# Kernel tuning notes

Hardware: AMD Instinct MI355X
Metric: run time of the kernel (lower is better)

Reference implementation:

```python
import jax, jax.numpy as jnp
import numpy as np

B, N, NTYPES, MN = 8, 1024, 2, 128
M = NTYPES * MN
BETA, M1, M2 = 8, 16, 4
NFEAT = M1 * M2
H = 128
NGHOST = 64
RMAX, RMIN = 6.0, 0.5
ENER_SHIFT = np.array([[-93.0], [-13.6]], dtype=np.float32)


def setup_inputs() -> dict:
    key = jax.random.key(0)
    ks = jax.random.split(key, 12)
    # displacement vectors with |r| in (1, Rmax-0.2)
    d = jax.random.normal(ks[0], (B, N, M, 3), jnp.float32)
    d = d / jnp.linalg.norm(d, axis=-1, keepdims=True)
    r = jax.random.uniform(ks[1], (B, N, M, 1), jnp.float32, 1.0, RMAX - 0.2)
    rvec = d * r
    list_neigh = jax.random.randint(ks[2], (B, N, NTYPES, MN), 1, N + NGHOST + 1).astype(jnp.int32)
    # sorted type map so per-type concat order matches original atom order
    Imagetype_map = jnp.concatenate([jnp.zeros(N // 2, jnp.int32), jnp.ones(N - N // 2, jnp.int32)])
    c_param = 0.1 * jax.random.normal(ks[3], (NTYPES, NTYPES, M1, BETA), jnp.float32)
    def w(k, shape):
        fan_in = shape[-2]
        return (1.0 / np.sqrt(fan_in)) * jax.random.normal(k, shape, jnp.float32)
    return {
        'list_neigh': list_neigh,
        'Imagetype_map': Imagetype_map,
        'rvec': rvec,
        'c_param': c_param,
        'W0': w(ks[4], (NTYPES, NFEAT, H)), 'b0': jnp.zeros((NTYPES, H), jnp.float32),
        'W1': w(ks[5], (NTYPES, H, H)),     'b1': jnp.zeros((NTYPES, H), jnp.float32),
        'W2': w(ks[6], (NTYPES, H, H)),     'b2': jnp.zeros((NTYPES, H), jnp.float32),
        'Wout': w(ks[7], (NTYPES, H, 1)),   'bout': jnp.asarray(ENER_SHIFT),
    }


def _cheb(u):
    # Chebyshev polynomials T_0..T_{BETA-1}, stacked on last axis
    Ts = [jnp.ones_like(u), u]
    for _ in range(2, BETA):
        Ts.append(2.0 * u * Ts[-1] - Ts[-2])
    return jnp.stack(Ts[:BETA], axis=-1)


def _features(rvec, Imagetype_map, c_param):
    r = jnp.linalg.norm(rvec, axis=-1)                      # (B,N,M)
    valid = r > 1e-6
    r_safe = jnp.where(valid, r, 1.0)
    span = RMAX - RMIN
    u = jnp.clip(2.0 * (r_safe - RMIN) / span - 1.0, -1.0, 1.0)
    fc = jnp.where(valid & (r_safe < RMAX),
                   0.5 * (jnp.cos(jnp.pi * (jnp.clip(r_safe, RMIN, RMAX) - RMIN) / span) + 1.0),
                   0.0)
    T = _cheb(u)                                            # (B,N,M,BETA)
    # per-pair Chebyshev coefficients c[type_i, type_j, m1, k]; neighbor type is the block index
    c_i = c_param[Imagetype_map]                            # (N, NTYPES, M1, BETA)
    c_pair = jnp.repeat(c_i, MN, axis=1)                    # (N, M, M1, BETA)
    g = jnp.einsum('bnmk,nmpk->bnmp', T, c_pair) * fc[..., None]   # (B,N,M,M1)
    unit = rvec / r_safe[..., None]
    q = jnp.concatenate([jnp.ones_like(r_safe)[..., None], unit], axis=-1)  # (B,N,M,4)
    q = q * valid[..., None]
    S = jnp.einsum('bnmp,bnma->bnpa', g, q) / M             # (B,N,M1,4)
    feat = jnp.einsum('bnpa,bnqa->bnpq', S, S[:, :, :M2])   # (B,N,M1,M2)
    return feat.reshape(feat.shape[0], feat.shape[1], NFEAT)


def _normalize(feat, Imagetype_map):
    # per-type StandardScaler over all feat values of atoms of that type (detached)
    means, stds = [], []
    for t in range(NTYPES):
        w = (Imagetype_map == t).astype(feat.dtype)         # (N,)
        cnt = w.sum() * feat.shape[0] * NFEAT
        mu = (feat * w[None, :, None]).sum() / cnt
        var = (((feat - mu) ** 2) * w[None, :, None]).sum() / (cnt - 1.0)
        means.append(mu)
        stds.append(jnp.sqrt(var))
    means = jax.lax.stop_gradient(jnp.stack(means))
    stds = jax.lax.stop_gradient(jnp.stack(stds))
    mt = means[Imagetype_map][None, :, None]
    st = stds[Imagetype_map][None, :, None]
    return (feat - mt) / st


def _fit(feat_n, Imagetype_map, W0, b0, W1, b1, W2, b2, Wout, bout):
    Ei = jnp.zeros(feat_n.shape[:2] + (1,), feat_n.dtype)
    for t in range(NTYPES):
        h = jnp.tanh(feat_n @ W0[t] + b0[t])
        h = jnp.tanh(h @ W1[t] + b1[t]) + h                 # resnet skip (equal dims)
        h = jnp.tanh(h @ W2[t] + b2[t]) + h
        e = h @ Wout[t] + bout[t]                           # (B,N,1)
        Ei = Ei + e * (Imagetype_map == t)[None, :, None]
    return Ei


def reference(list_neigh, Imagetype_map, rvec, c_param, W0, b0, W1, b1, W2, b2, Wout, bout):
    def ei_fn(rv):
        feat = _features(rv, Imagetype_map, c_param)
        feat_n = _normalize(feat, Imagetype_map)
        return _fit(feat_n, Imagetype_map, W0, b0, W1, b1, W2, b2, Wout, bout)

    Ei = ei_fn(rvec)                                        # (B,N,1)
    Etot = Ei.sum(axis=1)                                   # (B,1)

    # forces / virial: dE/d rij, scatter-add to center & neighbor atoms (incl. ghosts)
    dEdr = jax.grad(lambda rv: ei_fn(rv).sum())(rvec)       # (B,N,M,3)
    Force = jnp.zeros((B, N + NGHOST, 3), rvec.dtype)
    Force = Force.at[:, :N].add(dEdr.sum(axis=2))           # center atoms: F_i = +sum_j dE/drij
    nl = list_neigh.reshape(B, N, M)
    valid = nl > 0
    j = jnp.where(valid, nl - 1, 0)
    flat_idx = (jnp.arange(B)[:, None, None] * (N + NGHOST) + j).reshape(-1)
    contrib = jnp.where(valid[..., None], -dEdr, 0.0).reshape(-1, 3)
    Force = Force.reshape(-1, 3).at[flat_idx].add(contrib).reshape(B, N + NGHOST, 3)
    Virial = -jnp.einsum('bnma,bnmc->bac', rvec, dEdr).reshape(B, 9)
    return (Etot, Ei.squeeze(-1), Force, Virial)
```

## Files before the change

kernel.cpp:

```cpp
#include <hip/hip_runtime.h>
#include <math.h>

#define BB 8
#define NN 1024
#define MM 256
#define BETA 8
#define M1 16
#define NFEAT 64
#define HH 128
#define NTOT 1088
#define F3 (NTOT*3)
#define RMINf 0.5f
#define SPANf 5.5f
#define PIf 3.14159265358979323846f

#define OUT_EI 8
#define OUT_FORCE 8200
#define OUT_VIR 34312

#define NG2 128
#define AT2 (NN/NG2)

#define MT 16
#define AS0 68
#define AS1 132

#define FEAT_BLKS 2048

#define WS_S     0
#define WS_DF    (WS_S + 8192*64)
#define WS_FP    (WS_DF + 8192*64)
#define WS_STATP (WS_FP + BB*NG2*F3)
#define WS_VIRP  (WS_STATP + 8192*2)
#define WS_WTB   (WS_VIRP + BB*NG2*9)
#define WS_WB    (WS_WTB + 40960)
#define WT0_OFF  0
#define WT1_OFF  16384
#define WT2_OFF  49152

typedef __attribute__((ext_vector_type(8))) short bf8;
typedef __attribute__((ext_vector_type(4))) float f4;

__device__ __forceinline__ float ftanh(float x) {
  const float e = __expf(2.0f*x);
  return 1.0f - 2.0f/(e + 1.0f);
}
__device__ __forceinline__ short f2bs(float f) {
  unsigned u = __float_as_uint(f);
  return (short)((u + 0x7FFFu + ((u >> 16) & 1u)) >> 16);
}
__device__ __forceinline__ bf8 a_frag(const float* p) {
  bf8 a;
  #pragma unroll
  for (int i = 0; i < 8; ++i) a[i] = f2bs(p[i]);
  return a;
}
__device__ __forceinline__ f4 splat4(float v) {
  f4 r; r[0] = v; r[1] = v; r[2] = v; r[3] = v; return r;
}
__device__ __forceinline__ float dpp_wave_sum(float x) {
  x += __int_as_float(__builtin_amdgcn_update_dpp(0, __float_as_int(x), 0x111, 0xf, 0xf, true));
  x += __int_as_float(__builtin_amdgcn_update_dpp(0, __float_as_int(x), 0x112, 0xf, 0xf, true));
  x += __int_as_float(__builtin_amdgcn_update_dpp(0, __float_as_int(x), 0x114, 0xf, 0xf, true));
  x += __int_as_float(__builtin_amdgcn_update_dpp(0, __float_as_int(x), 0x118, 0xf, 0xf, true));
  x += __int_as_float(__builtin_amdgcn_update_dpp(0, __float_as_int(x), 0x142, 0xf, 0xf, true));
  x += __int_as_float(__builtin_amdgcn_update_dpp(0, __float_as_int(x), 0x143, 0xf, 0xf, true));
  return x;
}

__global__ __launch_bounds__(256) void k_feat(
    const float* __restrict__ rvec, const int* __restrict__ tmap,
    const float* __restrict__ c_param, float* __restrict__ S_ws,
    float* __restrict__ statp,
    const float* __restrict__ W0, const float* __restrict__ W1,
    const float* __restrict__ W2,
    unsigned short* __restrict__ wtb, unsigned short* __restrict__ wb)
{
  const int tid = threadIdx.x;
  if (blockIdx.x >= FEAT_BLKS) {
    const int idx = (blockIdx.x - FEAT_BLKS)*256 + tid;
    if (idx < 81920) {
      unsigned short v;
      if (idx < 16384) {
        const int t = idx >> 13, rem = idx & 8191;
        const int j = rem >> 6, f = rem & 63;
        v = (unsigned short)f2bs(W0[t*8192 + f*128 + j]);
      } else if (idx < 49152) {
        const int i = idx - 16384;
        const int t = i >> 14, rem = i & 16383;
        const int j = rem >> 7, f = rem & 127;
        v = (unsigned short)f2bs(W1[t*16384 + f*128 + j]);
      } else {
        const int i = idx - 49152;
        const int t = i >> 14, rem = i & 16383;
        const int j = rem >> 7, f = rem & 127;
        v = (unsigned short)f2bs(W2[t*16384 + f*128 + j]);
      }
      wtb[idx] = v;
    } else {
      const int k = idx - 81920;
      float src;
      if (k < 16384) src = W0[k];
      else if (k < 49152) src = W1[k - 16384];
      else src = W2[k - 49152];
      wb[k] = (unsigned short)f2bs(src);
    }
    return;
  }
  __shared__ float cA[512];
  __shared__ float Ubuf[4*64];
  __shared__ float Slds[4*64];
  cA[tid] = c_param[tid];
  cA[256 + tid] = c_param[256 + tid];
  __syncthreads();

  const int wave = tid >> 6, lane = tid & 63;
  const int bn = blockIdx.x*4 + wave;
  const int n = bn & (NN-1);
  const int ti = tmap[n];
  const float* rb = rvec + (size_t)bn*MM*3;

  #pragma unroll
  for (int half = 0; half < 2; ++half) {
    float acc[32];
    #pragma unroll
    for (int c = 0; c < 32; ++c) acc[c] = 0.f;
    #pragma unroll
    for (int s = 0; s < 2; ++s) {
      const int m = half*128 + s*64 + lane;
      const float x = rb[3*m], y = rb[3*m+1], z = rb[3*m+2];
      const float r = sqrtf(x*x + y*y + z*z);
      const float ir = 1.0f/r;
      const float ux = x*ir, uy = y*ir, uz = z*ir;
      float u = 2.0f*(r - RMINf)/SPANf - 1.0f;
      u = fminf(fmaxf(u, -1.0f), 1.0f);
      const float fc = 0.5f*(__cosf(PIf*(r - RMINf)/SPANf) + 1.0f);
      float tm2 = 1.0f, tm1 = u;
      acc[0] += fc;  acc[1] += fc*ux;  acc[2] += fc*uy;  acc[3] += fc*uz;
      {
        const float ft = fc*u;
        acc[4] += ft; acc[5] += ft*ux; acc[6] += ft*uy; acc[7] += ft*uz;
      }
      #pragma unroll
      for (int k = 2; k < BETA; ++k) {
        const float tk = 2.0f*u*tm1 - tm2;
        const float ft = fc*tk;
        acc[k*4+0] += ft;
        acc[k*4+1] += ft*ux;
        acc[k*4+2] += ft*uy;
        acc[k*4+3] += ft*uz;
        tm2 = tm1; tm1 = tk;
      }
    }
    #pragma unroll
    for (int c = 0; c < 32; ++c) acc[c] = dpp_wave_sum(acc[c]);
    if (lane == 63) {
      float* Uw = &Ubuf[wave*64 + half*32];
      #pragma unroll
      for (int c = 0; c < 32; ++c) Uw[c] = acc[c];
    }
  }
  {
    const int p = lane >> 2, a = lane & 3;
    const float* Uw = &Ubuf[wave*64];
    const float* cw = &cA[ti*256];
    float s = 0.f;
    #pragma unroll
    for (int tj = 0; tj < 2; ++tj)
      #pragma unroll
      for (int k = 0; k < 8; ++k)
        s += cw[tj*128 + p*8 + k] * Uw[tj*32 + k*4 + a];
    s *= (1.0f/(float)MM);
    Slds[wave*64 + lane] = s;
    S_ws[(size_t)bn*64 + lane] = s;
  }
  {
    const int p = lane >> 2, q = lane & 3;
    const float* Sw = &Slds[wave*64];
    float f = 0.f;
    #pragma unroll
    for (int a = 0; a < 4; ++a) f += Sw[p*4+a]*Sw[q*4+a];
    float fs = f, fss = f*f;
    for (int o = 32; o > 0; o >>= 1) { fs += __shfl_down(fs, o); fss += __shfl_down(fss, o); }
    if (lane == 0) { statp[bn*2+0] = fs; statp[bn*2+1] = fss; }
  }
}

__global__ __launch_bounds__(256) void k_mlp(
    const float* __restrict__ S_ws, const int* __restrict__ tmap,
    const float* __restrict__ statp,
    const unsigned short* __restrict__ wtb, const unsigned short* __restrict__ wb,
    const float* __restrict__ b0, const float* __restrict__ b1,
    const float* __restrict__ b2, const float* __restrict__ Wout,
    const float* __restrict__ bout,
    float* __restrict__ dfeat_ws, float* __restrict__ out)
{
  __shared__ float sl[MT*64];
  __shared__ float xb[MT*AS0];
  __shared__ float t0b[MT*AS1];
  __shared__ float h1b[MT*AS1];
  __shared__ float dzb[MT*AS1];
  __shared__ float es[MT];
  __shared__ float srd[8];
  __shared__ float muSd[2];
  const int tb = blockIdx.x;
  const int bn0 = tb*MT;
  const int tid = threadIdx.x;
  const int wave = tid >> 6, lane = tid & 63;
  const int quad = lane >> 4, nI = lane & 15;
  const int t = tmap[bn0 & (NN-1)];
  {
    const float4* src = (const float4*)(S_ws + (size_t)bn0*64);
    ((float4*)sl)[tid] = src[tid];
  }
  {
    float fs = 0.f, fss = 0.f;
    #pragma unroll 4
    for (int i = 0; i < 16; ++i) {
      const int e = i*256 + tid;
      const int b = e >> 9;
      const int n = t*512 + (e & 511);
      const float2 v = *(const float2*)&statp[((size_t)(b*NN + n))*2];
      fs += v.x; fss += v.y;
    }
    for (int o = 32; o > 0; o >>= 1) { fs += __shfl_down(fs, o); fss += __shfl_down(fss, o); }
    if ((tid & 63) == 0) { srd[(tid>>6)*2] = fs; srd[(tid>>6)*2+1] = fss; }
  }
  __syncthreads();
  if (tid == 0) {
    const float S1 = srd[0]+srd[2]+srd[4]+srd[6];
    const float S2 = srd[1]+srd[3]+srd[5]+srd[7];
    const float cnt = 512.0f * (float)BB * (float)NFEAT;
    const float mu = S1/cnt;
    const float var = (S2 - cnt*mu*mu)/(cnt - 1.0f);
    muSd[0] = mu; muSd[1] = sqrtf(fmaxf(var, 1e-20f));
  }
  __syncthreads();
  const float mu = muSd[0];
  const float inv_sd = 1.0f/muSd[1];
  #pragma unroll
  for (int i = 0; i < 4; ++i) {
    const int e = i*256 + tid;
    const int at = e >> 6, f = e & 63;
    const int p = f >> 2, q = f & 3;
    const float* Sr = &sl[at*64];
    float s = 0.f;
    #pragma unroll
    for (int a = 0; a < 4; ++a) s += Sr[p*4+a]*Sr[q*4+a];
    xb[at*AS0 + f] = (s - mu)*inv_sd;
  }
  __syncthreads();

  const int c0 = (wave*2+0)*16 + nI;
  const int c1 = (wave*2+1)*16 + nI;
  f4 acc0, acc1;

  acc0 = splat4(b0[t*HH + c0]);
  acc1 = splat4(b0[t*HH + c1]);
  {
    const unsigned short* B = wtb + WT0_OFF + t*8192;
    #pragma unroll
    for (int s = 0; s < 2; ++s) {
      const bf8 a  = a_frag(&xb[nI*AS0 + s*32 + quad*8]);
      const bf8 bA = *(const bf8*)&B[(size_t)c0*64 + s*32 + quad*8];
      const bf8 bB = *(const bf8*)&B[(size_t)c1*64 + s*32 + quad*8];
      acc0 = __builtin_amdgcn_mfma_f32_16x16x32_bf16(a, bA, acc0, 0, 0, 0);
      acc1 = __builtin_amdgcn_mfma_f32_16x16x32_bf16(a, bB, acc1, 0, 0, 0);
    }
  }
  #pragma unroll
  for (int r = 0; r < 4; ++r) {
    const int row = quad*4 + r;
    t0b[row*AS1 + c0] = ftanh(acc0[r]);
    t0b[row*AS1 + c1] = ftanh(acc1[r]);
  }
  __syncthreads();
  acc0 = splat4(b1[t*HH + c0]);
  acc1 = splat4(b1[t*HH + c1]);
  {
    const unsigned short* B = wtb + WT1_OFF + t*16384;
    #pragma unroll
    for (int s = 0; s < 4; ++s) {
      const bf8 a  = a_frag(&t0b[nI*AS1 + s*32 + quad*8]);
      const bf8 bA = *(const bf8*)&B[(size_t)c0*128 + s*32 + quad*8];
      const bf8 bB = *(const bf8*)&B[(size_t)c1*128 + s*32 + quad*8];
      acc0 = __builtin_amdgcn_mfma_f32_16x16x32_bf16(a, bA, acc0, 0, 0, 0);
      acc1 = __builtin_amdgcn_mfma_f32_16x16x32_bf16(a, bB, acc1, 0, 0, 0);
    }
  }
  #pragma unroll
  for (int r = 0; r < 4; ++r) {
    const int row = quad*4 + r;
    h1b[row*AS1 + c0] = ftanh(acc0[r]) + t0b[row*AS1 + c0];
    h1b[row*AS1 + c1] = ftanh(acc1[r]) + t0b[row*AS1 + c1];
  }
  __syncthreads();
  acc0 = splat4(b2[t*HH + c0]);
  acc1 = splat4(b2[t*HH + c1]);
  {
    const unsigned short* B = wtb + WT2_OFF + t*16384;
    #pragma unroll
    for (int s = 0; s < 4; ++s) {
      const bf8 a  = a_frag(&h1b[nI*AS1 + s*32 + quad*8]);
      const bf8 bA = *(const bf8*)&B[(size_t)c0*128 + s*32 + quad*8];
      const bf8 bB = *(const bf8*)&B[(size_t)c1*128 + s*32 + quad*8];
      acc0 = __builtin_amdgcn_mfma_f32_16x16x32_bf16(a, bA, acc0, 0, 0, 0);
      acc1 = __builtin_amdgcn_mfma_f32_16x16x32_bf16(a, bB, acc1, 0, 0, 0);
    }
  }
  #pragma unroll
  for (int r = 0; r < 4; ++r) {
    const int row = quad*4 + r;
    dzb[row*AS1 + c0] = acc0[r];
    dzb[row*AS1 + c1] = acc1[r];
  }
  __syncthreads();
  {
    const int at = tid >> 4, cb = (tid & 15)*8;
    const float* wop = Wout + t*HH;
    float ep = 0.f;
    #pragma unroll
    for (int j = 0; j < 8; ++j) {
      const int c = cb + j;
      const float z2 = dzb[at*AS1 + c];
      const float t2 = ftanh(z2);
      const float wo = wop[c];
      ep += (t2 + h1b[at*AS1 + c])*wo;
      dzb[at*AS1 + c] = wo*(1.0f - t2*t2);
    }
    ep += __shfl_down(ep, 8, 16);
    ep += __shfl_down(ep, 4, 16);
    ep += __shfl_down(ep, 2, 16);
    ep += __shfl_down(ep, 1, 16);
    if ((tid & 15) == 0) es[at] = ep;
  }
  __syncthreads();
  if (tid < MT) out[OUT_EI + bn0 + tid] = es[tid] + bout[t];

  {
    const float* wop = Wout + t*HH;
    acc0 = splat4(wop[c0]);
    acc1 = splat4(wop[c1]);
    const unsigned short* B = wb + WT2_OFF + t*16384;
    #pragma unroll
    for (int s = 0; s < 4; ++s) {
      const bf8 a  = a_frag(&dzb[nI*AS1 + s*32 + quad*8]);
      const bf8 bA = *(const bf8*)&B[(size_t)c0*128 + s*32 + quad*8];
      const bf8 bB = *(const bf8*)&B[(size_t)c1*128 + s*32 + quad*8];
      acc0 = __builtin_amdgcn_mfma_f32_16x16x32_bf16(a, bA, acc0, 0, 0, 0);
      acc1 = __builtin_amdgcn_mfma_f32_16x16x32_bf16(a, bB, acc1, 0, 0, 0);
    }
  }
  __syncthreads();
  float dh10[4], dh11[4];
  #pragma unroll
  for (int r = 0; r < 4; ++r) {
    const int row = quad*4 + r;
    dh10[r] = acc0[r]; dh11[r] = acc1[r];
    const float t1a = h1b[row*AS1 + c0] - t0b[row*AS1 + c0];
    const float t1b = h1b[row*AS1 + c1] - t0b[row*AS1 + c1];
    dzb[row*AS1 + c0] = acc0[r]*(1.0f - t1a*t1a);
    dzb[row*AS1 + c1] = acc1[r]*(1.0f - t1b*t1b);
  }
  __syncthreads();
  acc0[0]=dh10[0]; acc0[1]=dh10[1]; acc0[2]=dh10[2]; acc0[3]=dh10[3];
  acc1[0]=dh11[0]; acc1[1]=dh11[1]; acc1[2]=dh11[2]; acc1[3]=dh11[3];
  {
    const unsigned short* B = wb + WT1_OFF + t*16384;
    #pragma unroll
    for (int s = 0; s < 4; ++s) {
      const bf8 a  = a_frag(&dzb[nI*AS1 + s*32 + quad*8]);
      const bf8 bA = *(const bf8*)&B[(size_t)c0*128 + s*32 + quad*8];
      const bf8 bB = *(const bf8*)&B[(size_t)c1*128 + s*32 + quad*8];
      acc0 = __builtin_amdgcn_mfma_f32_16x16x32_bf16(a, bA, acc0, 0, 0, 0);
      acc1 = __builtin_amdgcn_mfma_f32_16x16x32_bf16(a, bB, acc1, 0, 0, 0);
    }
  }
  __syncthreads();
  #pragma unroll
  for (int r = 0; r < 4; ++r) {
    const int row = quad*4 + r;
    const float ta = t0b[row*AS1 + c0], tb = t0b[row*AS1 + c1];
    dzb[row*AS1 + c0] = acc0[r]*(1.0f - ta*ta);
    dzb[row*AS1 + c1] = acc1[r]*(1.0f - tb*tb);
  }
  __syncthreads();
  {
    const int cx = wave*16 + nI;
    acc0 = splat4(0.f);
    const unsigned short* B = wb + WT0_OFF + t*8192;
    #pragma unroll
    for (int s = 0; s < 4; ++s) {
      const bf8 a  = a_frag(&dzb[nI*AS1 + s*32 + quad*8]);
      const bf8 bA = *(const bf8*)&B[(size_t)cx*128 + s*32 + quad*8];
      acc0 = __builtin_amdgcn_mfma_f32_16x16x32_bf16(a, bA, acc0, 0, 0, 0);
    }
    #pragma unroll
    for (int r = 0; r < 4; ++r)
      dfeat_ws[(size_t)(bn0 + quad*4 + r)*64 + cx] = acc0[r]*inv_sd;
  }
}

__global__ __launch_bounds__(256, 4) void k_bwdsc(
    const float* __restrict__ rvec, const int* __restrict__ nlist,
    const int* __restrict__ tmap, const float* __restrict__ c_param,
    const float* __restrict__ S_ws, const float* __restrict__ dfeat_ws,
    float* __restrict__ fpart_ws, float* __restrict__ virp)
{
  __shared__ float c_lds[256];
  __shared__ float Sb[AT2*64];
  __shared__ float Db[AT2*64];
  __shared__ float dSb[AT2*64];
  __shared__ float Eb[AT2*64];
  __shared__ float fpart[F3];
  __shared__ float wredc[AT2*4*3];
  __shared__ float vred[4*9];
  const int blk = blockIdx.x;
  const int b = blk >> 7;
  const int g = blk & (NG2-1);
  const int n0 = g*AT2;
  const int tid = threadIdx.x;
  const int ti = tmap[n0];
  c_lds[tid] = c_param[ti*256 + tid];
  if (tid < 128) {
    const float4* s4 = (const float4*)(S_ws + ((size_t)b*NN + n0)*64);
    const float4* d4 = (const float4*)(dfeat_ws + ((size_t)b*NN + n0)*64);
    ((float4*)Sb)[tid] = s4[tid];
    ((float4*)Db)[tid] = d4[tid];
  }
  {
    const float4 z4 = {0.f, 0.f, 0.f, 0.f};
    for (int i = tid; i < F3/4; i += 256) ((float4*)fpart)[i] = z4;
  }
  __syncthreads();
  #pragma unroll
  for (int it = 0; it < 2; ++it) {
    const int idx = it*256 + tid;
    const int at = idx >> 6, f = idx & 63;
    const int i = f >> 2, a = f & 3;
    const float* Sr = &Sb[at*64];
    const float* Dr = &Db[at*64];
    float v = 0.f;
    #pragma unroll
    for (int q = 0; q < 4; ++q) v += Dr[i*4+q]*Sr[q*4+a];
    if (i < 4)
      for (int p = 0; p < 16; ++p) v += Dr[p*4+i]*Sr[p*4+a];
    dSb[idx] = v;
  }
  __syncthreads();
  #pragma unroll
  for (int it = 0; it < 2; ++it) {
    const int idx = it*256 + tid;
    const int at = idx >> 6, rem = idx & 63;
    const int tj = rem >> 5, a = (rem >> 3) & 3, k = rem & 7;
    float e = 0.f;
    #pragma unroll
    for (int p = 0; p < 16; ++p) e += dSb[at*64 + p*4 + a]*c_lds[tj*128 + p*8 + k];
    Eb[idx] = e;
  }
  __syncthreads();

  float vir[9];
  #pragma unroll
  for (int i = 0; i < 9; ++i) vir[i] = 0.f;
  const int wave = tid >> 6, lane = tid & 63;
  const int tjm = tid >> 7;
  const float dudr = 2.0f/SPANf;
  const float invM = 1.0f/(float)MM;

  const size_t rowbase = ((size_t)b*NN + n0)*MM;
  float px0, py0, pz0, px1, py1, pz1; int pnl0, pnl1;
  {
    const float* rp0 = rvec + (rowbase + tid)*3;
    const float* rp1 = rvec + (rowbase + MM + tid)*3;
    px0 = rp0[0]; py0 = rp0[1]; pz0 = rp0[2]; pnl0 = nlist[rowbase + tid];
    px1 = rp1[0]; py1 = rp1[1]; pz1 = rp1[2]; pnl1 = nlist[rowbase + MM + tid];
  }
  for (int a0 = 0; a0 < AT2; a0 += 2) {
    const float x0 = px0, y0 = py0, z0 = pz0; const int nl0 = pnl0;
    const float x1 = px1, y1 = py1, z1 = pz1; const int nl1 = pnl1;
    if (a0 + 2 < AT2) {
      const float* rp0 = rvec + (rowbase + (size_t)(a0+2)*MM + tid)*3;
      const float* rp1 = rvec + (rowbase + (size_t)(a0+3)*MM + tid)*3;
      px0 = rp0[0]; py0 = rp0[1]; pz0 = rp0[2];
      pnl0 = nlist[rowbase + (size_t)(a0+2)*MM + tid];
      px1 = rp1[0]; py1 = rp1[1]; pz1 = rp1[2];
      pnl1 = nlist[rowbase + (size_t)(a0+3)*MM + tid];
    }
    float Er0[32], Er1[32];
    {
      const float4* p0 = (const float4*)&Eb[a0*64 + tjm*32];
      const float4* p1 = (const float4*)&Eb[(a0+1)*64 + tjm*32];
      #pragma unroll
      for (int q = 0; q < 8; ++q) {
        const float4 v0 = p0[q], v1 = p1[q];
        Er0[q*4+0]=v0.x; Er0[q*4+1]=v0.y; Er0[q*4+2]=v0.z; Er0[q*4+3]=v0.w;
        Er1[q*4+0]=v1.x; Er1[q*4+1]=v1.y; Er1[q*4+2]=v1.z; Er1[q*4+3]=v1.w;
      }
    }
    const float r_0 = sqrtf(x0*x0 + y0*y0 + z0*z0);
    const float r_1 = sqrtf(x1*x1 + y1*y1 + z1*z1);
    const float ir0 = 1.0f/r_0, ir1 = 1.0f/r_1;
    const float ux0 = x0*ir0, uy0 = y0*ir0, uz0 = z0*ir0;
    const float ux1 = x1*ir1, uy1 = y1*ir1, uz1 = z1*ir1;
    float u0 = 2.0f*(r_0 - RMINf)/SPANf - 1.0f;
    float u1 = 2.0f*(r_1 - RMINf)/SPANf - 1.0f;
    u0 = fminf(fmaxf(u0, -1.0f), 1.0f);
    u1 = fminf(fmaxf(u1, -1.0f), 1.0f);
    float s0a, c0a, s1a, c1a;
    __sincosf(PIf*(r_0 - RMINf)/SPANf, &s0a, &c0a);
    __sincosf(PIf*(r_1 - RMINf)/SPANf, &s1a, &c1a);
    const float fc0 = 0.5f*(c0a + 1.0f), dfc0 = -0.5f*(PIf/SPANf)*s0a;
    const float fc1 = 0.5f*(c1a + 1.0f), dfc1 = -0.5f*(PIf/SPANf)*s1a;
    float ta0[4], tda0[4], ta1[4], tda1[4];
    #pragma unroll
    for (int aa = 0; aa < 4; ++aa) {
      ta0[aa]  = Er0[aa*8] + Er0[aa*8+1]*u0;
      tda0[aa] = Er0[aa*8+1];
      ta1[aa]  = Er1[aa*8] + Er1[aa*8+1]*u1;
      tda1[aa] = Er1[aa*8+1];
    }
    float t0m2 = 1.f, t0m1 = u0, d0m2 = 0.f, d0m1 = 1.f;
    float t1m2 = 1.f, t1m1 = u1, d1m2 = 0.f, d1m1 = 1.f;
    #pragma unroll
    for (int k = 2; k < BETA; ++k) {
      const float tk0 = 2.f*u0*t0m1 - t0m2;
      const float dk0 = 2.f*t0m1 + 2.f*u0*d0m1 - d0m2;
      const float tk1 = 2.f*u1*t1m1 - t1m2;
      const float dk1 = 2.f*t1m1 + 2.f*u1*d1m1 - d1m2;
      #pragma unroll
      for (int aa = 0; aa < 4; ++aa) {
        ta0[aa]  += Er0[aa*8+k]*tk0;
        tda0[aa] += Er0[aa*8+k]*dk0;
        ta1[aa]  += Er1[aa*8+k]*tk1;
        tda1[aa] += Er1[aa*8+k]*dk1;
      }
      t0m2 = t0m1; t0m1 = tk0; d0m2 = d0m1; d0m1 = dk0;
      t1m2 = t1m1; t1m1 = tk1; d1m2 = d1m1; d1m1 = dk1;
    }
    float A0 = dfc0*(ta0[0] + ux0*ta0[1] + uy0*ta0[2] + uz0*ta0[3])
             + fc0*dudr*(tda0[0] + ux0*tda0[1] + uy0*tda0[2] + uz0*tda0[3]);
    float A1 = dfc1*(ta1[0] + ux1*ta1[1] + uy1*ta1[2] + uz1*ta1[3])
             + fc1*dudr*(tda1[0] + ux1*tda1[1] + uy1*tda1[2] + uz1*tda1[3]);
    float q10 = fc0*ta0[1], q20 = fc0*ta0[2], q30 = fc0*ta0[3];
    float q11 = fc1*ta1[1], q21 = fc1*ta1[2], q31 = fc1*ta1[3];
    A0 *= invM; q10 *= invM; q20 *= invM; q30 *= invM;
    A1 *= invM; q11 *= invM; q21 *= invM; q31 *= invM;
    const float qu0 = q10*ux0 + q20*uy0 + q30*uz0;
    const float qu1 = q11*ux1 + q21*uy1 + q31*uz1;
    const float d00 = A0*ux0 + (q10 - qu0*ux0)*ir0;
    const float d01 = A0*uy0 + (q20 - qu0*uy0)*ir0;
    const float d02 = A0*uz0 + (q30 - qu0*uz0)*ir0;
    const float d10 = A1*ux1 + (q11 - qu1*ux1)*ir1;
    const float d11 = A1*uy1 + (q21 - qu1*uy1)*ir1;
    const float d12 = A1*uz1 + (q31 - qu1*uz1)*ir1;
    if (nl0 > 0) {
      const int j = nl0 - 1;
      atomicAdd(&fpart[j*3+0], -d00);
      atomicAdd(&fpart[j*3+1], -d01);
      atomicAdd(&fpart[j*3+2], -d02);
    }
    if (nl1 > 0) {
      const int j = nl1 - 1;
      atomicAdd(&fpart[j*3+0], -d10);
      atomicAdd(&fpart[j*3+1], -d11);
      atomicAdd(&fpart[j*3+2], -d12);
    }
    vir[0] -= x0*d00 + x1*d10; vir[1] -= x0*d01 + x1*d11; vir[2] -= x0*d02 + x1*d12;
    vir[3] -= y0*d00 + y1*d10; vir[4] -= y0*d01 + y1*d11; vir[5] -= y0*d02 + y1*d12;
    vir[6] -= z0*d00 + z1*d10; vir[7] -= z0*d01 + z1*d11; vir[8] -= z0*d02 + z1*d12;
    const float r00 = dpp_wave_sum(d00), r01 = dpp_wave_sum(d01), r02 = dpp_wave_sum(d02);
    const float r10 = dpp_wave_sum(d10), r11 = dpp_wave_sum(d11), r12 = dpp_wave_sum(d12);
    if (lane == 63) {
      wredc[(a0*4 + wave)*3 + 0] = r00;
      wredc[(a0*4 + wave)*3 + 1] = r01;
      wredc[(a0*4 + wave)*3 + 2] = r02;
      wredc[((a0+1)*4 + wave)*3 + 0] = r10;
      wredc[((a0+1)*4 + wave)*3 + 1] = r11;
      wredc[((a0+1)*4 + wave)*3 + 2] = r12;
    }
  }
  #pragma unroll
  for (int i = 0; i < 9; ++i) {
    const float v = dpp_wave_sum(vir[i]);
    if (lane == 63) vred[wave*9 + i] = v;
  }
  __syncthreads();
  if (tid < AT2*3) {
    const int at = tid/3, c = tid - at*3;
    const float v = wredc[(at*4+0)*3+c] + wredc[(at*4+1)*3+c]
                  + wredc[(at*4+2)*3+c] + wredc[(at*4+3)*3+c];
    atomicAdd(&fpart[(n0+at)*3 + c], v);
  }
  if (tid >= 64 && tid < 73) {
    const int i = tid - 64;
    virp[(size_t)blk*9 + i] = vred[i] + vred[9+i] + vred[18+i] + vred[27+i];
  }
  __syncthreads();
  {
    float* dst = fpart_ws + (size_t)blk*F3;
    for (int i = tid; i < F3/4; i += 256)
      ((float4*)dst)[i] = ((float4*)fpart)[i];
  }
}

__global__ __launch_bounds__(256) void k_reduce(
    const float* __restrict__ fpart_ws, const float* __restrict__ virp,
    float* __restrict__ out)
{
  __shared__ float comb[4*64];
  __shared__ float red[4];
  const int tid = threadIdx.x;
  const int blk = blockIdx.x;
  if (blk < 408) {
    const int el = tid & 63, gc = tid >> 6;
    const int e = blk*64 + el;
    const int b = e / F3;
    const int i = e - b*F3;
    const float* base = fpart_ws + (size_t)(b*NG2)*F3 + i;
    float s = 0.f;
    #pragma unroll 8
    for (int g = gc*32; g < gc*32 + 32; ++g) s += base[(size_t)g*F3];
    comb[gc*64 + el] = s;
    __syncthreads();
    if (tid < 64)
      out[OUT_FORCE + blk*64 + tid] = comb[tid] + comb[64+tid] + comb[128+tid] + comb[192+tid];
    return;
  }
  if (blk < 480) {
    const int vb = blk - 408;
    const int b = vb / 9, c = vb - (vb/9)*9;
    float v = (tid < NG2) ? virp[((size_t)(b*NG2 + tid))*9 + c] : 0.f;
    for (int o = 32; o > 0; o >>= 1) v += __shfl_down(v, o);
    if ((tid & 63) == 0) red[tid >> 6] = v;
    __syncthreads();
    if (tid == 0) out[OUT_VIR + vb] = red[0] + red[1];
    return;
  }
  const int b = blk - 480;
  float v = 0.f;
  #pragma unroll
  for (int k = 0; k < 4; ++k) v += out[OUT_EI + b*NN + k*256 + tid];
  for (int o = 32; o > 0; o >>= 1) v += __shfl_down(v, o);
  if ((tid & 63) == 0) red[tid >> 6] = v;
  __syncthreads();
  if (tid == 0) out[b] = red[0] + red[1] + red[2] + red[3];
}

extern "C" void kernel_launch(void* const* d_in, const int* in_sizes, int n_in,
                              void* d_out, int out_size, void* d_ws, size_t ws_size,
                              hipStream_t stream)
{
  const int*   nlist = (const int*)d_in[0];
  const int*   tmap  = (const int*)d_in[1];
  const float* rvec  = (const float*)d_in[2];
  const float* cpar  = (const float*)d_in[3];
  const float* W0 = (const float*)d_in[4];
  const float* b0 = (const float*)d_in[5];
  const float* W1 = (const float*)d_in[6];
  const float* b1 = (const float*)d_in[7];
  const float* W2 = (const float*)d_in[8];
  const float* b2 = (const float*)d_in[9];
  const float* Wout = (const float*)d_in[10];
  const float* bout = (const float*)d_in[11];
  float* out = (float*)d_out;
  float* ws = (float*)d_ws;
  float* S_ws   = ws + WS_S;
  float* df_ws  = ws + WS_DF;
  float* fpartw = ws + WS_FP;
  float* statp  = ws + WS_STATP;
  float* virp   = ws + WS_VIRP;
  unsigned short* wtb = (unsigned short*)(ws + WS_WTB);
  unsigned short* wb  = (unsigned short*)(ws + WS_WB);

  k_feat <<<FEAT_BLKS + 640, 256, 0, stream>>>(rvec, tmap, cpar, S_ws, statp,
                                               W0, W1, W2, wtb, wb);
  k_mlp  <<<(BB*NN)/MT, 256, 0, stream>>>(S_ws, tmap, statp, wtb, wb,
                                          b0, b1, b2, Wout, bout, df_ws, out);
  k_bwdsc<<<BB*NG2, 256, 0, stream>>>(rvec, nlist, tmap, cpar, S_ws, df_ws,
                                      fpartw, virp);
  k_reduce<<<488, 256, 0, stream>>>(fpartw, virp, out);
}
```

Baseline: 169.5 us.

## Replace partial-force workspace and reduce kernel with global atomics

Drops the k_reduce kernel and its per-block partial force and virial workspace. Each k_bwdsc block now atomically adds its full per-batch force buffer (3264 floats) and its virial into the output, and k_mlp atomically accumulates Etot per 16-atom tile. A memset of the output is added at the start. This removes the roughly 13 MB partial-buffer write and re-read plus one kernel launch, but brings heavy same-address atomic contention (128 blocks per batch adding to identical addresses) and makes float summation order nondeterministic.

```diff
diff --git a/kernel.cpp b/kernel.cpp
--- a/kernel.cpp
+++ b/kernel.cpp
@@ -29,10 +29,8 @@
 
 #define WS_S     0
 #define WS_DF    (WS_S + 8192*64)
-#define WS_FP    (WS_DF + 8192*64)
-#define WS_STATP (WS_FP + BB*NG2*F3)
-#define WS_VIRP  (WS_STATP + 8192*2)
-#define WS_WTB   (WS_VIRP + BB*NG2*9)
+#define WS_STATP (WS_DF + 8192*64)
+#define WS_WTB   (WS_STATP + 8192*2)
 #define WS_WB    (WS_WTB + 40960)
 #define WT0_OFF  0
 #define WT1_OFF  16384
@@ -336,6 +334,12 @@
   }
   __syncthreads();
   if (tid < MT) out[OUT_EI + bn0 + tid] = es[tid] + bout[t];
+  if (tid == 0) {
+    float s = 0.f;
+    #pragma unroll
+    for (int i = 0; i < MT; ++i) s += es[i];
+    atomicAdd(&out[bn0 >> 10], s + (float)MT*bout[t]);
+  }
 
   {
     const float* wop = Wout + t*HH;
@@ -405,7 +409,7 @@
     const float* __restrict__ rvec, const int* __restrict__ nlist,
     const int* __restrict__ tmap, const float* __restrict__ c_param,
     const float* __restrict__ S_ws, const float* __restrict__ dfeat_ws,
-    float* __restrict__ fpart_ws, float* __restrict__ virp)
+    float* __restrict__ out)
 {
   __shared__ float c_lds[256];
   __shared__ float Sb[AT2*64];
@@ -594,57 +598,15 @@
   }
   if (tid >= 64 && tid < 73) {
     const int i = tid - 64;
-    virp[(size_t)blk*9 + i] = vred[i] + vred[9+i] + vred[18+i] + vred[27+i];
-  }
-  __syncthreads();
-  {
-    float* dst = fpart_ws + (size_t)blk*F3;
-    for (int i = tid; i < F3/4; i += 256)
-      ((float4*)dst)[i] = ((float4*)fpart)[i];
-  }
-}
-
-__global__ __launch_bounds__(256) void k_reduce(
-    const float* __restrict__ fpart_ws, const float* __restrict__ virp,
-    float* __restrict__ out)
-{
-  __shared__ float comb[4*64];
-  __shared__ float red[4];
-  const int tid = threadIdx.x;
-  const int blk = blockIdx.x;
-  if (blk < 408) {
-    const int el = tid & 63, gc = tid >> 6;
-    const int e = blk*64 + el;
-    const int b = e / F3;
-    const int i = e - b*F3;
-    const float* base = fpart_ws + (size_t)(b*NG2)*F3 + i;
-    float s = 0.f;
-    #pragma unroll 8
-    for (int g = gc*32; g < gc*32 + 32; ++g) s += base[(size_t)g*F3];
-    comb[gc*64 + el] = s;
-    __syncthreads();
-    if (tid < 64)
-      out[OUT_FORCE + blk*64 + tid] = comb[tid] + comb[64+tid] + comb[128+tid] + comb[192+tid];
-    return;
-  }
-  if (blk < 480) {
-    const int vb = blk - 408;
-    const int b = vb / 9, c = vb - (vb/9)*9;
-    float v = (tid < NG2) ? virp[((size_t)(b*NG2 + tid))*9 + c] : 0.f;
-    for (int o = 32; o > 0; o >>= 1) v += __shfl_down(v, o);
-    if ((tid & 63) == 0) red[tid >> 6] = v;
-    __syncthreads();
-    if (tid == 0) out[OUT_VIR + vb] = red[0] + red[1];
-    return;
-  }
-  const int b = blk - 480;
-  float v = 0.f;
-  #pragma unroll
-  for (int k = 0; k < 4; ++k) v += out[OUT_EI + b*NN + k*256 + tid];
-  for (int o = 32; o > 0; o >>= 1) v += __shfl_down(v, o);
-  if ((tid & 63) == 0) red[tid >> 6] = v;
-  __syncthreads();
-  if (tid == 0) out[b] = red[0] + red[1] + red[2] + red[3];
+    atomicAdd(&out[OUT_VIR + b*9 + i],
+              vred[i] + vred[9+i] + vred[18+i] + vred[27+i]);
+  }
+  __syncthreads();
+  {
+    float* dst = out + OUT_FORCE + (size_t)b*F3;
+    for (int i = tid; i < F3; i += 256)
+      atomicAdd(&dst[i], fpart[i]);
+  }
 }
 
 extern "C" void kernel_launch(void* const* d_in, const int* in_sizes, int n_in,
@@ -667,17 +629,16 @@
   float* ws = (float*)d_ws;
   float* S_ws   = ws + WS_S;
   float* df_ws  = ws + WS_DF;
-  float* fpartw = ws + WS_FP;
   float* statp  = ws + WS_STATP;
-  float* virp   = ws + WS_VIRP;
   unsigned short* wtb = (unsigned short*)(ws + WS_WTB);
   unsigned short* wb  = (unsigned short*)(ws + WS_WB);
+
+  hipMemsetAsync(d_out, 0, (size_t)out_size, stream);
 
   k_feat <<<FEAT_BLKS + 640, 256, 0, stream>>>(rvec, tmap, cpar, S_ws, statp,
                                                W0, W1, W2, wtb, wb);
   k_mlp  <<<(BB*NN)/MT, 256, 0, stream>>>(S_ws, tmap, statp, wtb, wb,
                                           b0, b1, b2, Wout, bout, df_ws, out);
   k_bwdsc<<<BB*NG2, 256, 0, stream>>>(rvec, nlist, tmap, cpar, S_ws, df_ws,
-                                      fpartw, virp);
-  k_reduce<<<488, 256, 0, stream>>>(fpartw, virp, out);
-}
+                                      out);
+}
```

New measurement: 172.9 us. +2.0%, slower.
